# Performance work log

Hardware: AMD Instinct MI355X
Metric: run time of the kernel (lower is better)

Reference implementation:

```python
import jax, jax.numpy as jnp
import numpy as np

BN_EPS = 1e-5

def setup_inputs() -> dict:
    key = jax.random.key(0)
    ks = jax.random.split(key, 10)
    B, C, W, H = 4, 128, 32, 128
    Co = C // 2  # 64
    s_in = 1.0 / np.sqrt(C)
    s_out = 1.0 / np.sqrt(Co)
    return {
        "range_x": jax.random.normal(ks[0], (B, C, W, H), jnp.float32),
        "img": jax.random.normal(ks[1], (B, C, W, H), jnp.float32),
        "wq": jax.random.normal(ks[2], (Co, C), jnp.float32) * s_in,
        "bq": jax.random.normal(ks[3], (Co,), jnp.float32) * 0.01,
        "wk": jax.random.normal(ks[4], (Co, C), jnp.float32) * s_in,
        "bk": jax.random.normal(ks[5], (Co,), jnp.float32) * 0.01,
        "wv": jax.random.normal(ks[6], (Co, C), jnp.float32) * s_in,
        "bv": jax.random.normal(ks[7], (Co,), jnp.float32) * 0.01,
        "wc": jax.random.normal(ks[8], (C, Co), jnp.float32) * s_out,
        "bc": jax.random.normal(ks[9], (C,), jnp.float32) * 0.01,
        "bn_gamma": jnp.ones((C,), jnp.float32),
        "bn_beta": jnp.zeros((C,), jnp.float32),
        "bn_mean": jnp.zeros((C,), jnp.float32),
        "bn_var": jnp.ones((C,), jnp.float32),
    }

def reference(range_x, img, wq, bq, wk, bk, wv, bv, wc, bc, bn_gamma, bn_beta, bn_mean, bn_var):
    B, C, W, H = range_x.shape
    HW = W * H
    r = range_x.reshape(B, C, HW)  # [B,C,N]
    i = img.reshape(B, C, HW)
    # 1x1 convs == per-pixel linear projections
    q = jnp.einsum('oc,bcn->bno', wq, r) + bq            # [B,N,Co] (query from range)
    k = jnp.einsum('oc,bcn->bon', wk, i) + bk[None, :, None]  # [B,Co,N]
    corr = jnp.einsum('bno,bom->bnm', q, k)              # [B,N,N]
    attn = jax.nn.softmax(corr, axis=-1)
    v = jnp.einsum('oc,bcn->bon', wv, i) + bv[None, :, None]  # [B,Co,N]
    # out[b,o,n] = sum_m v[b,o,m] * attn[b,n,m]  (bmm(V, attn^T))
    out = jnp.einsum('bom,bnm->bon', v, attn)            # [B,Co,N]
    # channel_back: 1x1 conv -> BN (inference) -> ReLU
    y = jnp.einsum('co,bon->bcn', wc, out) + bc[None, :, None]
    inv = bn_gamma / jnp.sqrt(bn_var + BN_EPS)
    y = y * inv[None, :, None] + (bn_beta - bn_mean * inv)[None, :, None]
    y = jax.nn.relu(y)
    return img + y.reshape(B, C, W, H)
```

## Files before the change

### kernel.cpp

```cpp
#include <hip/hip_runtime.h>
#include <hip/hip_bf16.h>

typedef __attribute__((ext_vector_type(4))) float f32x4;
typedef __attribute__((ext_vector_type(8))) short s16x8;
typedef __attribute__((ext_vector_type(4))) short s16x4;

#define LOG2E 1.4426950408889634f

__device__ __forceinline__ ushort f2bf(float f){
  union { float f; unsigned u; } x; x.f = f;
  unsigned r = x.u + 0x7fffu + ((x.u >> 16) & 1u);
  return (ushort)(r >> 16);
}
__device__ __forceinline__ float bf2f(ushort h){
  union { unsigned u; float f; } x; x.u = ((unsigned)h) << 16;
  return x.f;
}

__device__ __forceinline__ float fexp2(float x){
#if __has_builtin(__builtin_amdgcn_exp2f)
  return __builtin_amdgcn_exp2f(x);
#else
  float r; asm("v_exp_f32 %0, %1" : "=v"(r) : "v"(x)); return r;
#endif
}

__device__ __forceinline__ void gload16(const void* g, void* l){
  __builtin_amdgcn_global_load_lds(
      (const __attribute__((address_space(1))) void*)g,
      (__attribute__((address_space(3))) void*)l, 16, 0, 0);
}

#if __has_builtin(__builtin_amdgcn_mfma_f32_16x16x16bf16_1k)
__device__ __forceinline__ f32x4 mfma16(s16x4 a, s16x4 b, f32x4 c){
  return __builtin_amdgcn_mfma_f32_16x16x16bf16_1k(a, b, c, 0, 0, 0);
}
#elif __has_builtin(__builtin_amdgcn_mfma_f32_16x16x16_bf16)
__device__ __forceinline__ f32x4 mfma16(s16x4 a, s16x4 b, f32x4 c){
  return __builtin_amdgcn_mfma_f32_16x16x16_bf16(a, b, c, 0, 0, 0);
}
#else
__device__ __forceinline__ f32x4 mfma16(s16x4 a, s16x4 b, f32x4 c){
  f32x4 d;
  asm volatile("v_mfma_f32_16x16x16_bf16 %0, %1, %2, %3\n\ts_nop 7\n\ts_nop 7"
               : "=v"(d) : "v"(a), "v"(b), "v"(c));
  return d;
}
#endif

__global__ __launch_bounds__(256, 4) void proj_qkv(
    const float* __restrict__ xr, const float* __restrict__ xi,
    const float* __restrict__ wq, const float* __restrict__ wk,
    const float* __restrict__ wv,
    const float* __restrict__ bq, const float* __restrict__ bk,
    const float* __restrict__ bv,
    ushort* __restrict__ Qh, ushort* __restrict__ Ql,
    ushort* __restrict__ Kh, ushort* __restrict__ Vt)
{
  __shared__ __align__(16) float xL[128*64];
  const int tid = threadIdx.x;
  const int idx = blockIdx.x;
  const int oq  = idx & 3;
  const int nt  = (idx >> 2) & 63;
  const int b   = idx >> 8;
  const int n0  = nt << 6;
  const int lane = tid & 63;
  const int w    = tid >> 6;
  const int l15  = lane & 15;
  const int g    = lane >> 4;
  const int obase = oq << 4;

  #define STAGE_X(src)                                                    \
  {                                                                       \
    const float* xs = (src) + (size_t)b*524288 + n0;                      \
    _Pragma("unroll")                                                     \
    for (int j = 0; j < 8; ++j){                                          \
      int row = j*16 + (tid >> 4);                                        \
      int ch  = tid & 15;                                                 \
      gload16(xs + (size_t)row*4096 + ch*4, xL + j*1024 + w*256);         \
    }                                                                     \
  }
  #define BUILD_FRAGS(fh, fl)                                             \
  {                                                                       \
    const int px = w*16 + l15;                                            \
    _Pragma("unroll")                                                     \
    for (int kc = 0; kc < 4; ++kc){                                       \
      _Pragma("unroll")                                                   \
      for (int j = 0; j < 8; ++j){                                        \
        int r = kc*32 + g*8 + j;                                          \
        float a = xL[r*64 + px];                                          \
        ushort h = f2bf(a);                                               \
        fh[kc][j] = (short)h;                                             \
        fl[kc][j] = (short)f2bf(a - bf2f(h));                             \
      }                                                                   \
    }                                                                     \
  }
  #define LOAD_WFRAGS(wp, wh, wl4)                                        \
  {                                                                       \
    _Pragma("unroll")                                                     \
    for (int kc = 0; kc < 4; ++kc){                                       \
      const float* src = (wp) + (obase + l15)*128 + kc*32 + g*8;          \
      f32x4 a0 = *(const f32x4*)(src);                                    \
      f32x4 a1 = *(const f32x4*)(src + 4);                                \
      _Pragma("unroll")                                                   \
      for (int e = 0; e < 4; ++e){                                        \
        ushort h0 = f2bf(a0[e]);                                          \
        wh[kc][e]   = (short)h0;                                          \
        wl4[kc][e]  = (short)f2bf(a0[e] - bf2f(h0));                      \
        ushort h1 = f2bf(a1[e]);                                          \
        wh[kc][4+e]  = (short)h1;                                         \
        wl4[kc][4+e] = (short)f2bf(a1[e] - bf2f(h1));                     \
      }                                                                   \
    }                                                                     \
  }

  STAGE_X(xr);
  __syncthreads();
  {
    s16x8 xh[4], xl4[4];
    BUILD_FRAGS(xh, xl4);
    s16x8 wfh[4], wfl[4];
    LOAD_WFRAGS(wq, wfh, wfl);
    f32x4 acc = {0.f,0.f,0.f,0.f};
    #pragma unroll
    for (int kc = 0; kc < 4; ++kc){
      acc = __builtin_amdgcn_mfma_f32_16x16x32_bf16(xh[kc],  wfh[kc], acc, 0,0,0);
      acc = __builtin_amdgcn_mfma_f32_16x16x32_bf16(xl4[kc], wfh[kc], acc, 0,0,0);
      acc = __builtin_amdgcn_mfma_f32_16x16x32_bf16(xh[kc],  wfl[kc], acc, 0,0,0);
    }
    float bqv = bq[obase + l15];
    #pragma unroll
    for (int r = 0; r < 4; ++r){
      float q = (acc[r] + bqv) * LOG2E;
      ushort hi = f2bf(q);
      size_t a = (size_t)(b*4096 + n0 + w*16 + g*4 + r)*64 + obase + l15;
      Qh[a] = hi; Ql[a] = f2bf(q - bf2f(hi));
    }
  }
  __syncthreads();

  STAGE_X(xi);
  __syncthreads();
  {
    s16x8 xh[4], xl4[4];
    BUILD_FRAGS(xh, xl4);
    {
      s16x8 wfh[4], wfl[4];
      LOAD_WFRAGS(wk, wfh, wfl);
      f32x4 acc = {0.f,0.f,0.f,0.f};
      #pragma unroll
      for (int kc = 0; kc < 4; ++kc){
        acc = __builtin_amdgcn_mfma_f32_16x16x32_bf16(xh[kc],  wfh[kc], acc, 0,0,0);
        acc = __builtin_amdgcn_mfma_f32_16x16x32_bf16(xl4[kc], wfh[kc], acc, 0,0,0);
        acc = __builtin_amdgcn_mfma_f32_16x16x32_bf16(xh[kc],  wfl[kc], acc, 0,0,0);
      }
      float bkv = bk[obase + l15];
      #pragma unroll
      for (int r = 0; r < 4; ++r){
        size_t a = (size_t)(b*4096 + n0 + w*16 + g*4 + r)*64 + obase + l15;
        Kh[a] = f2bf(acc[r] + bkv);
      }
    }
    {
      s16x8 wfh[4], wfl[4];
      LOAD_WFRAGS(wv, wfh, wfl);
      f32x4 acc = {0.f,0.f,0.f,0.f};
      #pragma unroll
      for (int kc = 0; kc < 4; ++kc){
        acc = __builtin_amdgcn_mfma_f32_16x16x32_bf16(wfh[kc], xh[kc],  acc, 0,0,0);
        acc = __builtin_amdgcn_mfma_f32_16x16x32_bf16(wfl[kc], xh[kc],  acc, 0,0,0);
        acc = __builtin_amdgcn_mfma_f32_16x16x32_bf16(wfh[kc], xl4[kc], acc, 0,0,0);
      }
      #pragma unroll
      for (int r = 0; r < 4; ++r){
        int o = obase + g*4 + r;
        float v = acc[r] + bv[o];
        Vt[(size_t)(b*64 + o)*4096 + n0 + w*16 + l15] = f2bf(v);
      }
    }
  }
  #undef STAGE_X
  #undef BUILD_FRAGS
  #undef LOAD_WFRAGS
}

__global__ __launch_bounds__(256, 5) void flash_attn(
    const ushort* __restrict__ Qh, const ushort* __restrict__ Ql,
    const ushort* __restrict__ Kh, const ushort* __restrict__ Vt,
    float* __restrict__ Opart, float* __restrict__ Mst,
    float* __restrict__ Lst)
{
  __shared__ __align__(16) ushort khL[2][4096];
  __shared__ __align__(16) ushort vL[2][4096];

  const int tid  = threadIdx.x;
  const int idx  = blockIdx.x;
  const int xcd  = idx & 7;
  const int rest = idx >> 3;
  const int b    = xcd >> 1;
  const int ks   = ((xcd & 1) << 1) | (rest >> 6);
  const int qt   = rest & 63;
  const int lane = tid & 63;
  const int w    = tid >> 6;
  const int l15  = lane & 15;
  const int g    = lane >> 4;
  const int qrow = qt*64 + w*16;
  const int kv0  = ks << 10;
  const int srow = lane >> 2;
  const int sg   = lane & 3;
  const int sgs  = sg ^ ((srow >> 1) & 3);

  const size_t qoff = ((size_t)(b*4096 + qrow + l15))*64 + g*8;
  s16x8 qh0 = *(const s16x8*)(Qh + qoff);
  s16x8 qh1 = *(const s16x8*)(Qh + qoff + 32);
  s16x8 ql0 = *(const s16x8*)(Ql + qoff);
  s16x8 ql1 = *(const s16x8*)(Ql + qoff + 32);

  const char* KhB = (const char*)(Kh + (size_t)b*4096*64);
  const char* VB  = (const char*)(Vt + (size_t)b*64*4096);

  f32x4 o_acc[4];
  #pragma unroll
  for (int ot=0;ot<4;++ot) o_acc[ot] = (f32x4){0.f,0.f,0.f,0.f};
  float m_run = -1e30f, l_run = 0.f;

  #define STAGE_KV(kvb, bi)                                               \
  {                                                                       \
    size_t kr = (size_t)((kvb) + w*16 + srow)*128 + sgs*16;               \
    char* kd = (char*)khL[bi] + w*2048;                                   \
    gload16(KhB + kr,      kd);                                           \
    gload16(KhB + kr + 64, kd + 1024);                                    \
    size_t vr = (size_t)(w*16 + srow)*8192 + (size_t)(kvb)*2 + sgs*16;    \
    char* vd = (char*)vL[bi] + w*2048;                                    \
    gload16(VB + vr,      vd);                                            \
    gload16(VB + vr + 64, vd + 1024);                                     \
  }

  STAGE_KV(kv0, 0);
  __syncthreads();

  const int swz = (l15 >> 1) & 3;
  const int kfrag = l15*64 + (g ^ swz)*16;

  for (int t = 0; t < 16; ++t){
    const int cb = t & 1;

    if (t < 15){
      STAGE_KV(kv0 + (t+1)*64, cb ^ 1);
    }

    f32x4 s[4];
    #pragma unroll
    for (int ct=0; ct<4; ++ct){
      const char* kb = (const char*)khL[cb] + ct*2048;
      s16x8 kh0 = *(const s16x8*)(kb + kfrag);
      s16x8 kh1 = *(const s16x8*)(kb + 1024 + kfrag);
      f32x4 acc = {0.f,0.f,0.f,0.f};
      acc = __builtin_amdgcn_mfma_f32_16x16x32_bf16(kh0, ql0, acc, 0, 0, 0);
      acc = __builtin_amdgcn_mfma_f32_16x16x32_bf16(kh1, ql1, acc, 0, 0, 0);
      acc = __builtin_amdgcn_mfma_f32_16x16x32_bf16(kh0, qh0, acc, 0, 0, 0);
      acc = __builtin_amdgcn_mfma_f32_16x16x32_bf16(kh1, qh1, acc, 0, 0, 0);
      s[ct] = acc;
    }

    float mx = s[0][0];
    #pragma unroll
    for (int ct=0;ct<4;++ct){
      #pragma unroll
      for (int r=0;r<4;++r) mx = fmaxf(mx, s[ct][r]);
    }
    mx = fmaxf(mx, __shfl_xor(mx, 16));
    mx = fmaxf(mx, __shfl_xor(mx, 32));
    if (!__all(mx <= m_run + 8.0f)){
      float mn = fmaxf(m_run, mx);
      float sc = fexp2(m_run - mn);
      m_run = mn;
      l_run *= sc;
      #pragma unroll
      for (int ot=0;ot<4;++ot) o_acc[ot] *= sc;
    }
    float rs = 0.f;
    s16x4 pbf[4];
    #pragma unroll
    for (int ct=0;ct<4;++ct){
      #pragma unroll
      for (int r=0;r<4;++r){
        float p = fexp2(s[ct][r] - m_run);
        rs += p;
        pbf[ct][r] = (short)f2bf(p);
      }
    }
    rs += __shfl_xor(rs, 16);
    rs += __shfl_xor(rs, 32);
    l_run += rs;

    #pragma unroll
    for (int ot=0; ot<4; ++ot){
      const char* vbase = (const char*)vL[cb] + ot*2048 + l15*64;
      #pragma unroll
      for (int ct=0; ct<4; ++ct){
        int chunk = (((ct & 1) << 1) + (g >> 1)) ^ swz;
        s16x4 av = *(const s16x4*)(vbase + (ct>>1)*1024 + chunk*16 + (g&1)*8);
        o_acc[ot] = mfma16(av, pbf[ct], o_acc[ot]);
      }
    }

    __syncthreads();
  }
  #undef STAGE_KV

  float* ep = (float*)((char*)vL + (size_t)w*4096);
  #pragma unroll
  for (int ot=0;ot<4;++ot){
    int dw = l15*64 + ((ot*16 + g*4) ^ ((l15 & 7) << 2));
    *(f32x4*)(ep + dw) = o_acc[ot];
  }
  __syncthreads();
  {
    const int q4  = lane >> 2;
    const int seg = lane & 3;
    float* Ob = Opart + ((size_t)(ks*4 + b)*4096 + qrow)*64;
    #pragma unroll
    for (int c=0;c<4;++c){
      int o0 = seg*16 + c*4;
      f32x4 vv = *(const f32x4*)(ep + q4*64 + (o0 ^ ((q4 & 7) << 2)));
      *(f32x4*)(Ob + (size_t)q4*64 + o0) = vv;
    }
  }
  if (lane < 16){
    Mst[(size_t)(ks*4 + b)*4096 + qrow + lane] = m_run;
    Lst[(size_t)(ks*4 + b)*4096 + qrow + lane] = l_run;
  }
}

__global__ __launch_bounds__(256) void final_proj(
    const float* __restrict__ Opart, const float* __restrict__ Mst,
    const float* __restrict__ Lst, const float* __restrict__ wc,
    const float* __restrict__ bc, const float* __restrict__ gm,
    const float* __restrict__ bt, const float* __restrict__ mu,
    const float* __restrict__ vr, const float* __restrict__ img,
    float* __restrict__ out)
{
  __shared__ float ol[64*64];
  __shared__ float scl[4][64];
  const int tid = threadIdx.x;
  const int idx = blockIdx.x;
  const int cs  = idx & 3;
  const int nt  = (idx >> 2) & 63;
  const int b   = idx >> 8;
  const int n0  = nt << 6;

  if (tid < 64){
    size_t rid = (size_t)b*4096 + n0 + tid;
    float m0 = Mst[0*16384 + rid], m1 = Mst[1*16384 + rid];
    float m2 = Mst[2*16384 + rid], m3 = Mst[3*16384 + rid];
    float mm = fmaxf(fmaxf(m0,m1), fmaxf(m2,m3));
    float s0 = fexp2(m0-mm), s1 = fexp2(m1-mm);
    float s2 = fexp2(m2-mm), s3 = fexp2(m3-mm);
    float li = s0*Lst[0*16384+rid] + s1*Lst[1*16384+rid]
             + s2*Lst[2*16384+rid] + s3*Lst[3*16384+rid];
    float inv = 1.0f / li;
    scl[0][tid] = s0*inv; scl[1][tid] = s1*inv;
    scl[2][tid] = s2*inv; scl[3][tid] = s3*inv;
  }
  __syncthreads();

  {
    const size_t base = ((size_t)b*4096 + n0)*64;
    for (int j=0;j<16;++j){
      int flat = tid + (j << 8);
      int n = flat >> 6, o = flat & 63;
      float v = Opart[0*(size_t)16384*64 + base + flat] * scl[0][n]
              + Opart[1*(size_t)16384*64 + base + flat] * scl[1][n]
              + Opart[2*(size_t)16384*64 + base + flat] * scl[2][n]
              + Opart[3*(size_t)16384*64 + base + flat] * scl[3][n];
      ol[(o << 6) + (n ^ (o & 31))] = v;
    }
  }
  __syncthreads();

  const int lane = tid & 63;
  const int w = __builtin_amdgcn_readfirstlane(tid >> 6);
  const int c0 = (cs << 5) + (w << 3);

  float acc[8];
  #pragma unroll
  for (int cc=0;cc<8;++cc) acc[cc] = 0.f;

  for (int o=0;o<64;++o){
    float v = ol[(o << 6) + (lane ^ (o & 31))];
    #pragma unroll
    for (int cc=0;cc<8;++cc)
      acc[cc] = fmaf(wc[(c0+cc)*64 + o], v, acc[cc]);
  }

  #pragma unroll
  for (int cc=0;cc<8;++cc){
    int c = c0 + cc;
    float inv = gm[c] * rsqrtf(vr[c] + 1e-5f);
    float sh  = bt[c] - mu[c]*inv;
    float y = (acc[cc] + bc[c]) * inv + sh;
    y = fmaxf(y, 0.f);
    size_t gi = ((size_t)(b*128 + c))*4096 + n0 + lane;
    out[gi] = img[gi] + y;
  }
}

extern "C" void kernel_launch(void* const* d_in, const int* in_sizes, int n_in,
                              void* d_out, int out_size, void* d_ws, size_t ws_size,
                              hipStream_t stream)
{
  const float* xr = (const float*)d_in[0];
  const float* xi = (const float*)d_in[1];
  const float* wq = (const float*)d_in[2];
  const float* bq = (const float*)d_in[3];
  const float* wk = (const float*)d_in[4];
  const float* bk = (const float*)d_in[5];
  const float* wv = (const float*)d_in[6];
  const float* bv = (const float*)d_in[7];
  const float* wc = (const float*)d_in[8];
  const float* bc = (const float*)d_in[9];
  const float* gm = (const float*)d_in[10];
  const float* bt = (const float*)d_in[11];
  const float* mu = (const float*)d_in[12];
  const float* vr = (const float*)d_in[13];
  float* out = (float*)d_out;

  const size_t SZ = (size_t)4*4096*64;
  ushort* Qhw = (ushort*)d_ws;
  ushort* Qlw = Qhw + SZ;
  ushort* Khw = Qlw + SZ;
  ushort* Vtw = Khw + SZ;
  float*  Ow  = (float*)(Vtw + SZ);
  float*  Mw  = Ow + (size_t)16*4096*64;
  float*  Lw  = Mw + (size_t)16*4096;

  proj_qkv  <<<1024, 256, 0, stream>>>(xr, xi, wq, wk, wv, bq, bk, bv,
                                       Qhw, Qlw, Khw, Vtw);
  flash_attn<<<1024, 256, 0, stream>>>(Qhw, Qlw, Khw, Vtw, Ow, Mw, Lw);
  final_proj<<<1024, 256, 0, stream>>>(Ow, Mw, Lw, wc, bc, gm, bt, mu, vr, xi, out);
}
```

Baseline: 87.81 us.

## Triple-buffer KV staging in flash attention and halve final_proj grid

```diff
diff --git a/kernel.cpp b/kernel.cpp
--- a/kernel.cpp
+++ b/kernel.cpp
@@ -184,14 +184,14 @@
   #undef LOAD_WFRAGS
 }
 
-__global__ __launch_bounds__(256, 5) void flash_attn(
+__global__ __launch_bounds__(256, 4) void flash_attn(
     const ushort* __restrict__ Qh, const ushort* __restrict__ Ql,
     const ushort* __restrict__ Kh, const ushort* __restrict__ Vt,
     float* __restrict__ Opart, float* __restrict__ Mst,
     float* __restrict__ Lst)
 {
-  __shared__ __align__(16) ushort khL[2][4096];
-  __shared__ __align__(16) ushort vL[2][4096];
+  __shared__ __align__(16) ushort khL[3][4096];
+  __shared__ __align__(16) ushort vL[3][4096];
 
   const int tid  = threadIdx.x;
   const int idx  = blockIdx.x;
@@ -236,79 +236,88 @@
     gload16(VB + vr + 64, vd + 1024);                                     \
   }
 
-  STAGE_KV(kv0, 0);
-  __syncthreads();
-
   const int swz = (l15 >> 1) & 3;
   const int kfrag = l15*64 + (g ^ swz)*16;
 
-  for (int t = 0; t < 16; ++t){
-    const int cb = t & 1;
-
-    if (t < 15){
-      STAGE_KV(kv0 + (t+1)*64, cb ^ 1);
-    }
-
-    f32x4 s[4];
-    #pragma unroll
-    for (int ct=0; ct<4; ++ct){
-      const char* kb = (const char*)khL[cb] + ct*2048;
-      s16x8 kh0 = *(const s16x8*)(kb + kfrag);
-      s16x8 kh1 = *(const s16x8*)(kb + 1024 + kfrag);
-      f32x4 acc = {0.f,0.f,0.f,0.f};
-      acc = __builtin_amdgcn_mfma_f32_16x16x32_bf16(kh0, ql0, acc, 0, 0, 0);
-      acc = __builtin_amdgcn_mfma_f32_16x16x32_bf16(kh1, ql1, acc, 0, 0, 0);
-      acc = __builtin_amdgcn_mfma_f32_16x16x32_bf16(kh0, qh0, acc, 0, 0, 0);
-      acc = __builtin_amdgcn_mfma_f32_16x16x32_bf16(kh1, qh1, acc, 0, 0, 0);
-      s[ct] = acc;
-    }
-
-    float mx = s[0][0];
-    #pragma unroll
-    for (int ct=0;ct<4;++ct){
-      #pragma unroll
-      for (int r=0;r<4;++r) mx = fmaxf(mx, s[ct][r]);
-    }
-    mx = fmaxf(mx, __shfl_xor(mx, 16));
-    mx = fmaxf(mx, __shfl_xor(mx, 32));
-    if (!__all(mx <= m_run + 8.0f)){
-      float mn = fmaxf(m_run, mx);
-      float sc = fexp2(m_run - mn);
-      m_run = mn;
-      l_run *= sc;
-      #pragma unroll
-      for (int ot=0;ot<4;++ot) o_acc[ot] *= sc;
-    }
-    float rs = 0.f;
-    s16x4 pbf[4];
-    #pragma unroll
-    for (int ct=0;ct<4;++ct){
-      #pragma unroll
-      for (int r=0;r<4;++r){
-        float p = fexp2(s[ct][r] - m_run);
-        rs += p;
-        pbf[ct][r] = (short)f2bf(p);
-      }
-    }
-    rs += __shfl_xor(rs, 16);
-    rs += __shfl_xor(rs, 32);
-    l_run += rs;
-
-    #pragma unroll
-    for (int ot=0; ot<4; ++ot){
-      const char* vbase = (const char*)vL[cb] + ot*2048 + l15*64;
-      #pragma unroll
-      for (int ct=0; ct<4; ++ct){
-        int chunk = (((ct & 1) << 1) + (g >> 1)) ^ swz;
-        s16x4 av = *(const s16x4*)(vbase + (ct>>1)*1024 + chunk*16 + (g&1)*8);
-        o_acc[ot] = mfma16(av, pbf[ct], o_acc[ot]);
-      }
-    }
-
-    __syncthreads();
-  }
+  #define COMPUTE(bi)                                                     \
+  {                                                                       \
+    f32x4 s[4];                                                           \
+    _Pragma("unroll")                                                     \
+    for (int ct=0; ct<4; ++ct){                                           \
+      const char* kb = (const char*)khL[bi] + ct*2048;                    \
+      s16x8 kh0 = *(const s16x8*)(kb + kfrag);                            \
+      s16x8 kh1 = *(const s16x8*)(kb + 1024 + kfrag);                     \
+      f32x4 acc = {0.f,0.f,0.f,0.f};                                      \
+      acc = __builtin_amdgcn_mfma_f32_16x16x32_bf16(kh0, ql0, acc,0,0,0); \
+      acc = __builtin_amdgcn_mfma_f32_16x16x32_bf16(kh1, ql1, acc,0,0,0); \
+      acc = __builtin_amdgcn_mfma_f32_16x16x32_bf16(kh0, qh0, acc,0,0,0); \
+      acc = __builtin_amdgcn_mfma_f32_16x16x32_bf16(kh1, qh1, acc,0,0,0); \
+      s[ct] = acc;                                                        \
+    }                                                                     \
+    float mx = s[0][0];                                                   \
+    _Pragma("unroll")                                                     \
+    for (int ct=0;ct<4;++ct){                                             \
+      _Pragma("unroll")                                                   \
+      for (int r=0;r<4;++r) mx = fmaxf(mx, s[ct][r]);                     \
+    }                                                                     \
+    mx = fmaxf(mx, __shfl_xor(mx, 16));                                   \
+    mx = fmaxf(mx, __shfl_xor(mx, 32));                                   \
+    if (!__all(mx <= m_run + 8.0f)){                                      \
+      float mn = fmaxf(m_run, mx);                                        \
+      float sc = fexp2(m_run - mn);                                       \
+      m_run = mn;                                                         \
+      l_run *= sc;                                                        \
+      _Pragma("unroll")                                                   \
+      for (int ot=0;ot<4;++ot) o_acc[ot] *= sc;                           \
+    }                                                                     \
+    float rs = 0.f;                                                       \
+    s16x4 pbf[4];                                                         \
+    _Pragma("unroll")                                                     \
+    for (int ct=0;ct<4;++ct){                                             \
+      _Pragma("unroll")                                                   \
+      for (int r=0;r<4;++r){                                              \
+        float p = fexp2(s[ct][r] - m_run);                                \
+        rs += p;                                                          \
+        pbf[ct][r] = (short)f2bf(p);                                      \
+      }                                                                   \
+    }                                                                     \
+    rs += __shfl_xor(rs, 16);                                             \
+    rs += __shfl_xor(rs, 32);                                             \
+    l_run += rs;                                                          \
+    _Pragma("unroll")                                                     \
+    for (int ot=0; ot<4; ++ot){                                           \
+      const char* vbase = (const char*)vL[bi] + ot*2048 + l15*64;         \
+      _Pragma("unroll")                                                   \
+      for (int ct=0; ct<4; ++ct){                                         \
+        int chunk = (((ct & 1) << 1) + (g >> 1)) ^ swz;                   \
+        s16x4 av = *(const s16x4*)(vbase + (ct>>1)*1024 + chunk*16        \
+                                   + (g&1)*8);                            \
+        o_acc[ot] = mfma16(av, pbf[ct], o_acc[ot]);                       \
+      }                                                                   \
+    }                                                                     \
+  }
+
+  STAGE_KV(kv0, 0);
+  STAGE_KV(kv0 + 64, 1);
+
+  for (int t = 0; t < 15; ++t){
+    asm volatile("s_waitcnt vmcnt(4)" ::: "memory");
+    __builtin_amdgcn_s_barrier();
+    __builtin_amdgcn_sched_barrier(0);
+    if (t < 14){
+      STAGE_KV(kv0 + (t+2)*64, (t+2) % 3);
+    }
+    const int bi = t % 3;
+    COMPUTE(bi);
+  }
+  asm volatile("s_waitcnt vmcnt(0)" ::: "memory");
+  __builtin_amdgcn_s_barrier();
+  __builtin_amdgcn_sched_barrier(0);
+  COMPUTE(0);
   #undef STAGE_KV
-
+  #undef COMPUTE
+
+  __syncthreads();
   float* ep = (float*)((char*)vL + (size_t)w*4096);
   #pragma unroll
   for (int ot=0;ot<4;++ot){
@@ -345,9 +354,9 @@
   __shared__ float scl[4][64];
   const int tid = threadIdx.x;
   const int idx = blockIdx.x;
-  const int cs  = idx & 3;
-  const int nt  = (idx >> 2) & 63;
-  const int b   = idx >> 8;
+  const int cs  = idx & 1;
+  const int nt  = (idx >> 1) & 63;
+  const int b   = idx >> 7;
   const int n0  = nt << 6;
 
   if (tid < 64){
@@ -381,21 +390,21 @@
 
   const int lane = tid & 63;
   const int w = __builtin_amdgcn_readfirstlane(tid >> 6);
-  const int c0 = (cs << 5) + (w << 3);
-
-  float acc[8];
+  const int c0 = (cs << 6) + (w << 4);
+
+  float acc[16];
   #pragma unroll
-  for (int cc=0;cc<8;++cc) acc[cc] = 0.f;
+  for (int cc=0;cc<16;++cc) acc[cc] = 0.f;
 
   for (int o=0;o<64;++o){
     float v = ol[(o << 6) + (lane ^ (o & 31))];
     #pragma unroll
-    for (int cc=0;cc<8;++cc)
+    for (int cc=0;cc<16;++cc)
       acc[cc] = fmaf(wc[(c0+cc)*64 + o], v, acc[cc]);
   }
 
   #pragma unroll
-  for (int cc=0;cc<8;++cc){
+  for (int cc=0;cc<16;++cc){
     int c = c0 + cc;
     float inv = gm[c] * rsqrtf(vr[c] + 1e-5f);
     float sh  = bt[c] - mu[c]*inv;
@@ -438,5 +447,5 @@
   proj_qkv  <<<1024, 256, 0, stream>>>(xr, xi, wq, wk, wv, bq, bk, bv,
                                        Qhw, Qlw, Khw, Vtw);
   flash_attn<<<1024, 256, 0, stream>>>(Qhw, Qlw, Khw, Vtw, Ow, Mw, Lw);
-  final_proj<<<1024, 256, 0, stream>>>(Ow, Mw, Lw, wc, bc, gm, bt, mu, vr, xi, out);
-}
+  final_proj<<<512,  256, 0, stream>>>(Ow, Mw, Lw, wc, bc, gm, bt, mu, vr, xi, out);
+}
```

After: 91.52 us. +4.2%, slower.
